# Kernel tuning notes

Hardware: AMD Instinct MI355X
Metric: run time of the kernel (lower is better)

Reference implementation:

```python
import jax, jax.numpy as jnp
from jax import lax
import numpy as np

STATE_DIM = 64
CHANNELS = 128
SEQ_LEN = 4096
BATCH = 16
DT_MIN, DT_MAX = 1e-3, 1e-1


def hippo(n):
    # HiPPO-LegS construction, matching the torch staticmethod
    ar = jnp.arange(n, dtype=jnp.float32)
    P = jnp.sqrt(1.0 + 2.0 * ar)
    A = P[:, None] * P[None, :]
    A = jnp.tril(A) - jnp.diag(ar)
    B = jnp.sqrt(2.0 * ar + 1.0)
    return -A, B[:, None]


def setup_inputs() -> dict:
    key = jax.random.key(0)
    k_u, k_c = jax.random.split(key)
    A, B = hippo(STATE_DIM)
    # xavier_normal_ for C: std = sqrt(2/(fan_in+fan_out))
    std = float(np.sqrt(2.0 / (CHANNELS + STATE_DIM)))
    C = jax.random.normal(k_c, (CHANNELS, STATE_DIM), dtype=jnp.float32) * std
    D = jnp.ones((CHANNELS, 1), dtype=jnp.float32)
    # deterministic dt at log-midpoint of [dt_min, dt_max]
    dt = jnp.exp(jnp.array([(np.log(DT_MIN) + np.log(DT_MAX)) / 2.0], dtype=jnp.float32))
    u = jax.random.normal(k_u, (BATCH, SEQ_LEN), dtype=jnp.float32)
    return {"u": u, "A": A, "B": B, "C": C, "D": D, "dt": dt}


def reference(u, A, B, C, D, dt):
    # Training-path forward of LinearStateSpaceLayer (conv-kernel construction + conv1d)
    b, L = u.shape
    n = A.shape[0]
    dt_s = dt[0]
    I = jnp.eye(n, dtype=A.dtype)
    BL = jnp.linalg.inv(I - 0.5 * dt_s * A)            # bilinear discretization
    A_bar = BL @ (I + 0.5 * dt_s * A)                  # (n, n)
    B_bar = (BL * dt_s) @ B                            # (n, 1)

    # kernel k[j] = C @ A_bar^j @ B_bar for j = 0..L-1, via a scan of matvecs
    def step(v, _):
        return A_bar @ v, v
    _, vs = lax.scan(step, B_bar[:, 0], None, length=L)  # (L, n), vs[j] = A_bar^j B_bar
    k_causal = vs @ C.T                                  # (L, channels)
    # torch ordering: k_conv[c, 0, i] = C A_bar^{L-1-i} B_bar = k_causal[L-1-i, c]
    k_conv = k_causal[::-1].T[:, None, :]                # (channels, 1, L)

    # torch F.conv1d is cross-correlation; lax conv_general_dilated matches
    y = lax.conv_general_dilated(
        u[:, None, :], k_conv,
        window_strides=(1,), padding=[(L - 1, L - 1)],
        dimension_numbers=("NCH", "OIH", "NCH"),
    )[:, :, :L]                                          # (b, channels, L)

    # skip term: (u.unsqueeze(-1) @ D.T).transpose(-1,-2) == u[b,t] * D[c,0]
    y = y + u[:, None, :] * D[None, :, :]                # (b, channels, L)
    return y
```

## Files before the change

### kernel.cpp

```cpp
#include <hip/hip_runtime.h>

#define NS   64
#define CH   128
#define LSEQ 4096
#define NB   16
#define SCH  64
#define MCH  64
#define ST   68
#define CP   128

#define WS_ABAR 0
#define WS_A16  4096
#define WS_VS   8192
#define WS_BBAR 12288

#define X0_IDX(b, m) (((size_t)(b) * CH) * LSEQ + (size_t)(m) * SCH)

#define P_VSS  0
#define P_XCW  1024
#define P_XBS  1280
#define P_PLE  1536
#define P_PART 1792
#define P_A16  2048

#define FMA44(av, bv)                                                          \
    a0.x += av.x * bv.x; a0.y += av.x * bv.y; a0.z += av.x * bv.z; a0.w += av.x * bv.w; \
    a1.x += av.y * bv.x; a1.y += av.y * bv.y; a1.z += av.y * bv.z; a1.w += av.y * bv.w; \
    a2.x += av.z * bv.x; a2.y += av.z * bv.y; a2.z += av.z * bv.z; a2.w += av.z * bv.w; \
    a3.x += av.w * bv.x; a3.y += av.w * bv.y; a3.z += av.w * bv.z; a3.w += av.w * bv.w;

template<bool WT>
__device__ __forceinline__ void mm_square(const float* __restrict__ cm,
                                          const float* __restrict__ cmt,
                                          float* __restrict__ nm,
                                          float* __restrict__ nmt, int e) {
    const int l = e & 63;
    const int si0 = 16 * ((e >> 6) & 3) + 4 * (l >> 4);
    const int sj0 = 4 * (l & 15);
    float4 a0 = {0,0,0,0}, a1 = {0,0,0,0}, a2 = {0,0,0,0}, a3 = {0,0,0,0};
#pragma unroll 4
    for (int k = 0; k < NS; k += 4) {
        float4 av0 = *(const float4*)&cmt[(k + 0) * ST + si0];
        float4 bv0 = *(const float4*)&cm [(k + 0) * ST + sj0];
        float4 av1 = *(const float4*)&cmt[(k + 1) * ST + si0];
        float4 bv1 = *(const float4*)&cm [(k + 1) * ST + sj0];
        float4 av2 = *(const float4*)&cmt[(k + 2) * ST + si0];
        float4 bv2 = *(const float4*)&cm [(k + 2) * ST + sj0];
        float4 av3 = *(const float4*)&cmt[(k + 3) * ST + si0];
        float4 bv3 = *(const float4*)&cm [(k + 3) * ST + sj0];
        FMA44(av0, bv0)
        FMA44(av1, bv1)
        FMA44(av2, bv2)
        FMA44(av3, bv3)
    }
    *(float4*)&nm[(si0 + 0) * ST + sj0] = a0;
    *(float4*)&nm[(si0 + 1) * ST + sj0] = a1;
    *(float4*)&nm[(si0 + 2) * ST + sj0] = a2;
    *(float4*)&nm[(si0 + 3) * ST + sj0] = a3;
    if (WT) {
        float4 t0 = {a0.x, a1.x, a2.x, a3.x};
        float4 t1 = {a0.y, a1.y, a2.y, a3.y};
        float4 t2 = {a0.z, a1.z, a2.z, a3.z};
        float4 t3 = {a0.w, a1.w, a2.w, a3.w};
        *(float4*)&nmt[(sj0 + 0) * ST + si0] = t0;
        *(float4*)&nmt[(sj0 + 1) * ST + si0] = t1;
        *(float4*)&nmt[(sj0 + 2) * ST + si0] = t2;
        *(float4*)&nmt[(sj0 + 3) * ST + si0] = t3;
    }
}

template<int R>
__device__ __forceinline__ void horner_step(const float* __restrict__ Acol,
                                            const float* __restrict__ xle,
                                            const float* __restrict__ Hprev,
                                            float* __restrict__ Hcur, int e) {
    const int g = e >> 4, i0 = 4 * (e & 15);
    const float* bp = (R == 1) ? &xle[(4 * g) * NS] : &Hprev[g * ST];
    float4 acc = *(const float4*)&xle[(4 * g + R) * NS + i0];
#pragma unroll 8
    for (int k = 0; k < NS; ++k) {
        float4 av = *(const float4*)&Acol[k * ST + i0];
        float bk = bp[k];
        acc.x = fmaf(av.x, bk, acc.x); acc.y = fmaf(av.y, bk, acc.y);
        acc.z = fmaf(av.z, bk, acc.z); acc.w = fmaf(av.w, bk, acc.w);
    }
    *(float4*)&Hcur[g * ST + i0] = acc;
}

__device__ __forceinline__ void inner_step(const float* __restrict__ Acol,
                                           const float* __restrict__ xle,
                                           float* __restrict__ stash, int r, int e) {
    const int g = e >> 4, i0 = 4 * (e & 15);
    const int mp = 4 * g + r - 1;
    float4 acc = *(const float4*)&xle[mp * NS + i0];
    const float* xp = &stash[mp * ST];
#pragma unroll 8
    for (int k = 0; k < NS; ++k) {
        float4 av = *(const float4*)&Acol[k * ST + i0];
        float xk = xp[k];
        acc.x = fmaf(av.x, xk, acc.x); acc.y = fmaf(av.y, xk, acc.y);
        acc.z = fmaf(av.z, xk, acc.z); acc.w = fmaf(av.w, xk, acc.w);
    }
    *(float4*)&stash[(mp + 1) * ST + i0] = acc;
}

__global__ __launch_bounds__(512) void k_sb(const float* __restrict__ u,
                                            const float* __restrict__ A,
                                            const float* __restrict__ Bv,
                                            const float* __restrict__ dtp,
                                            float* __restrict__ ws,
                                            float* __restrict__ out) {
    __shared__ __align__(16) float Mrow[NS * ST];
    __shared__ __align__(16) float Mcol[(NS + 1) * ST];
    __shared__ __align__(16) float Nrow[NS * ST];
    __shared__ __align__(16) float Ncol[NS * ST];
    __shared__ __align__(16) float VT[NS * ST];
    __shared__ __align__(16) float uT[NS * ST];
    __shared__ __align__(16) float vsS[NS * NS];
    __shared__ __align__(16) float xleS[MCH * NS];
    __shared__ __align__(16) float part[2][4 * NS];
    __shared__ __align__(16) float bcol[NS];
    __shared__ float rdiag[NS], xcS[NS];
    float* const stash = uT;
    float* const Hb0 = vsS;
    float* const Hb1 = vsS + 16 * ST;
    const int tid = threadIdx.x;
    const int b = blockIdx.x;
    const float dt = dtp[0];
    const float hdt = 0.5f * dt;

    for (int o = tid; o < NS * NS; o += 512) {
        int i = o >> 6, k = o & 63;
        float a = A[o];
        float d = (i == k) ? 1.0f : 0.0f;
        Nrow[i * ST + k] = d - hdt * a;
        Ncol[k * ST + i] = d + hdt * a;
    }
    if (tid < NS) {
        bcol[tid]  = dt * Bv[tid];
        rdiag[tid] = 1.0f / (1.0f - hdt * A[tid * NS + tid]);
    }
    __syncthreads();

    {
        const int jj = tid & 63;
#pragma unroll
        for (int rep = 0; rep < 2; ++rep) {
            const int m0 = 4 * (tid >> 6) + 32 * rep;
            float4 v;
            v.x = u[b * LSEQ + (m0 + 0) * SCH + 63 - jj];
            v.y = u[b * LSEQ + (m0 + 1) * SCH + 63 - jj];
            v.z = u[b * LSEQ + (m0 + 2) * SCH + 63 - jj];
            v.w = u[b * LSEQ + (m0 + 3) * SCH + 63 - jj];
            *(float4*)&uT[jj * ST + m0] = v;
        }
    }

    if (tid <= NS) {
        float xr[NS];
        const float* t2b = (tid < NS) ? &Ncol[tid * ST] : bcol;
#pragma unroll
        for (int I = 0; I < 16; ++I) {
            const int i0 = 4 * I;
            float4 t2 = *(const float4*)&t2b[i0];
            float a0 = t2.x, a1 = t2.y, a2 = t2.z, a3 = t2.w;
#pragma unroll
            for (int k = 0; k < i0; k += 4) {
                float4 n0 = *(const float4*)&Nrow[(i0 + 0) * ST + k];
                float4 n1 = *(const float4*)&Nrow[(i0 + 1) * ST + k];
                float4 n2 = *(const float4*)&Nrow[(i0 + 2) * ST + k];
                float4 n3 = *(const float4*)&Nrow[(i0 + 3) * ST + k];
                a0 -= n0.x * xr[k] + n0.y * xr[k + 1] + n0.z * xr[k + 2] + n0.w * xr[k + 3];
                a1 -= n1.x * xr[k] + n1.y * xr[k + 1] + n1.z * xr[k + 2] + n1.w * xr[k + 3];
                a2 -= n2.x * xr[k] + n2.y * xr[k + 1] + n2.z * xr[k + 2] + n2.w * xr[k + 3];
                a3 -= n3.x * xr[k] + n3.y * xr[k + 1] + n3.z * xr[k + 2] + n3.w * xr[k + 3];
            }
            float4 rd  = *(const float4*)&rdiag[i0];
            float4 nb1 = *(const float4*)&Nrow[(i0 + 1) * ST + i0];
            float4 nb2 = *(const float4*)&Nrow[(i0 + 2) * ST + i0];
            float4 nb3 = *(const float4*)&Nrow[(i0 + 3) * ST + i0];
            float x0 = a0 * rd.x;
            float x1 = (a1 - nb1.x * x0) * rd.y;
            float x2 = (a2 - nb2.x * x0 - nb2.y * x1) * rd.z;
            float x3 = (a3 - nb3.x * x0 - nb3.y * x1 - nb3.z * x2) * rd.w;
            xr[i0 + 0] = x0; xr[i0 + 1] = x1; xr[i0 + 2] = x2; xr[i0 + 3] = x3;
        }
        float* xrow = &Mcol[tid * ST];
#pragma unroll
        for (int k = 0; k < NS; k += 4) {
            float4 v = {xr[k], xr[k + 1], xr[k + 2], xr[k + 3]};
            *(float4*)&xrow[k] = v;
        }
    }
    __syncthreads();

    if (tid < 256) {
        const int i0 = 4 * (tid >> 4), j0 = 4 * (tid & 15);
        float4 r0 = *(const float4*)&Mcol[(j0 + 0) * ST + i0];
        float4 r1 = *(const float4*)&Mcol[(j0 + 1) * ST + i0];
        float4 r2 = *(const float4*)&Mcol[(j0 + 2) * ST + i0];
        float4 r3 = *(const float4*)&Mcol[(j0 + 3) * ST + i0];
        float4 w0 = {r0.x, r1.x, r2.x, r3.x};
        float4 w1 = {r0.y, r1.y, r2.y, r3.y};
        float4 w2 = {r0.z, r1.z, r2.z, r3.z};
        float4 w3 = {r0.w, r1.w, r2.w, r3.w};
        *(float4*)&Mrow[(i0 + 0) * ST + j0] = w0;
        *(float4*)&Mrow[(i0 + 1) * ST + j0] = w1;
        *(float4*)&Mrow[(i0 + 2) * ST + j0] = w2;
        *(float4*)&Mrow[(i0 + 3) * ST + j0] = w3;
        if (b == 0) {
            *(float4*)&ws[WS_ABAR + (i0 + 0) * NS + j0] = w0;
            *(float4*)&ws[WS_ABAR + (i0 + 1) * NS + j0] = w1;
            *(float4*)&ws[WS_ABAR + (i0 + 2) * NS + j0] = w2;
            *(float4*)&ws[WS_ABAR + (i0 + 3) * NS + j0] = w3;
        }
    }
    if (b == 0 && tid < 16)
        *(float4*)&ws[WS_BBAR + 4 * tid] = *(const float4*)&Mcol[NS * ST + 4 * tid];
    if (tid < NS) VT[tid * ST + 0] = Mcol[NS * ST + tid];
    __syncthreads();

    float *cm = Mrow, *cmt = Mcol, *nm = Nrow, *nmt = Ncol;
    for (int s = 1; s <= 6; ++s) {
        if (tid < 256) {
            mm_square<true>(cm, cmt, nm, nmt, tid);
        } else {
            const int e = tid - 256;
            if (s == 1) {
                if (e < NS) {
                    float sum = 0.f;
#pragma unroll 8
                    for (int k = 0; k < NS; ++k) sum += cmt[k * ST + e] * VT[k * ST + 0];
                    VT[e * ST + 1] = sum;
                }
            } else if (s == 2) {
                if (e < 2 * NS) {
                    const int i = e & 63, j = e >> 6;
                    float sum = 0.f;
#pragma unroll 8
                    for (int k = 0; k < NS; ++k) sum += cmt[k * ST + i] * VT[k * ST + j];
                    VT[i * ST + 2 + j] = sum;
                }
            } else {
                const int mexp = 1 << (s - 1);
                if (e < 4 * mexp) {
                    const int vi = 4 * (e & 15), vj = 4 * (e >> 4);
                    float4 a0 = {0,0,0,0}, a1 = {0,0,0,0}, a2 = {0,0,0,0}, a3 = {0,0,0,0};
#pragma unroll 4
                    for (int k = 0; k < NS; k += 2) {
                        float4 av  = *(const float4*)&cmt[k * ST + vi];
                        float4 bv  = *(const float4*)&VT [k * ST + vj];
                        float4 av2 = *(const float4*)&cmt[(k + 1) * ST + vi];
                        float4 bv2 = *(const float4*)&VT [(k + 1) * ST + vj];
                        FMA44(av, bv)
                        FMA44(av2, bv2)
                    }
                    *(float4*)&VT[(vi + 0) * ST + vj + mexp] = a0;
                    *(float4*)&VT[(vi + 1) * ST + vj + mexp] = a1;
                    *(float4*)&VT[(vi + 2) * ST + vj + mexp] = a2;
                    *(float4*)&VT[(vi + 3) * ST + vj + mexp] = a3;
                }
            }
        }
        __syncthreads();
        { float* t = cm; cm = nm; nm = t; t = cmt; cmt = nmt; nmt = t; }
        if (s == 4 && b == 0) {
            for (int o = tid; o < (NS * NS) / 4; o += 512) {
                int r = o >> 4, c4 = (o & 15) * 4;
                *(float4*)&ws[WS_A16 + r * NS + c4] = *(const float4*)&cm[r * ST + c4];
            }
        }
    }

    if (tid < 256) {
        const int i0 = 4 * (tid >> 4), j0 = 4 * (tid & 15);
        float4 v0 = *(const float4*)&VT[(i0 + 0) * ST + j0];
        float4 v1 = *(const float4*)&VT[(i0 + 1) * ST + j0];
        float4 v2 = *(const float4*)&VT[(i0 + 2) * ST + j0];
        float4 v3 = *(const float4*)&VT[(i0 + 3) * ST + j0];
        float4 w0 = {v0.x, v1.x, v2.x, v3.x};
        float4 w1 = {v0.y, v1.y, v2.y, v3.y};
        float4 w2 = {v0.z, v1.z, v2.z, v3.z};
        float4 w3 = {v0.w, v1.w, v2.w, v3.w};
        *(float4*)&vsS[(j0 + 0) * NS + i0] = w0;
        *(float4*)&vsS[(j0 + 1) * NS + i0] = w1;
        *(float4*)&vsS[(j0 + 2) * NS + i0] = w2;
        *(float4*)&vsS[(j0 + 3) * NS + i0] = w3;
        if (b == 0) {
            *(float4*)&ws[WS_VS + (j0 + 0) * NS + i0] = w0;
            *(float4*)&ws[WS_VS + (j0 + 1) * NS + i0] = w1;
            *(float4*)&ws[WS_VS + (j0 + 2) * NS + i0] = w2;
            *(float4*)&ws[WS_VS + (j0 + 3) * NS + i0] = w3;
        }
    } else {
        mm_square<true>(Mrow, Mcol, Nrow, Ncol, tid - 256);
    }
    __syncthreads();

    if (tid < 256) {
        const int ig = tid & 15, mg = tid >> 4;
        float4 a0 = {0,0,0,0}, a1 = {0,0,0,0}, a2 = {0,0,0,0}, a3 = {0,0,0,0};
#pragma unroll 4
        for (int j = 0; j < NS; j += 2) {
            float4 am  = *(const float4*)&uT[j * ST + 4 * mg];
            float4 bi  = *(const float4*)&vsS[j * NS + 4 * ig];
            float4 am2 = *(const float4*)&uT[(j + 1) * ST + 4 * mg];
            float4 bi2 = *(const float4*)&vsS[(j + 1) * NS + 4 * ig];
            FMA44(am, bi)
            FMA44(am2, bi2)
        }
        *(float4*)&xleS[(4 * mg + 0) * NS + 4 * ig] = a0;
        *(float4*)&xleS[(4 * mg + 1) * NS + 4 * ig] = a1;
        *(float4*)&xleS[(4 * mg + 2) * NS + 4 * ig] = a2;
        *(float4*)&xleS[(4 * mg + 3) * NS + 4 * ig] = a3;
    } else {
        mm_square<false>(Nrow, Ncol, VT, VT, tid - 256);
    }
    __syncthreads();

    float4 a256[4];
    if (tid < 256) {
        const int i = tid & 63, q = tid >> 6;
#pragma unroll
        for (int kq = 0; kq < 4; ++kq)
            a256[kq] = *(const float4*)&VT[i * ST + 16 * q + 4 * kq];
        horner_step<1>(Mcol, xleS, Hb0, Hb0, tid);
    } else if (tid < 320) {
        xcS[tid - 256] = 0.f;
        stash[tid - 256] = 0.f;
    }
    __syncthreads();
    if (tid < 256) horner_step<2>(Mcol, xleS, Hb0, Hb1, tid);
    __syncthreads();
    if (tid < 256) horner_step<3>(Mcol, xleS, Hb1, Hb0, tid);
    __syncthreads();

    {
        const int i = tid & 63, q = (tid >> 6) & 3;
        for (int g = 0; g < 15; ++g) {
            if (tid < 256) {
                float4 t0 = *(const float4*)(xcS + 16 * q + 0);
                float4 t1 = *(const float4*)(xcS + 16 * q + 4);
                float4 t2 = *(const float4*)(xcS + 16 * q + 8);
                float4 t3 = *(const float4*)(xcS + 16 * q + 12);
                float s = a256[0].x * t0.x + a256[0].y * t0.y + a256[0].z * t0.z + a256[0].w * t0.w
                        + a256[1].x * t1.x + a256[1].y * t1.y + a256[1].z * t1.z + a256[1].w * t1.w
                        + a256[2].x * t2.x + a256[2].y * t2.y + a256[2].z * t2.z + a256[2].w * t2.w
                        + a256[3].x * t3.x + a256[3].y * t3.y + a256[3].z * t3.z + a256[3].w * t3.w;
                part[g & 1][q * 64 + i] = s;
            }
            __syncthreads();
            if (tid < 256) {
                float xn = part[g & 1][i] + part[g & 1][64 + i] + part[g & 1][128 + i]
                         + part[g & 1][192 + i] + Hb0[g * ST + i];
                xcS[i] = xn;
                stash[(4 * g + 4) * ST + i] = xn;
            }
        }
    }
    __syncthreads();

    for (int r = 1; r <= 3; ++r) {
        if (tid < 256) inner_step(Mcol, xleS, stash, r, tid);
        __syncthreads();
    }

    {
        const int m = tid >> 3, t8 = (tid & 7) * 8;
        float4 o1 = *(const float4*)&stash[m * ST + t8];
        float4 o2 = *(const float4*)&stash[m * ST + t8 + 4];
        *(float4*)&out[X0_IDX(b, m) + t8]     = o1;
        *(float4*)&out[X0_IDX(b, m) + t8 + 4] = o2;
    }
}

__global__ __launch_bounds__(256) void k_main2(const float* __restrict__ u,
                                               const float* __restrict__ Cm,
                                               const float* __restrict__ Dv,
                                               const float* __restrict__ ws,
                                               float* __restrict__ out) {
    __shared__ __align__(16) float Xl[NS * ST];
    __shared__ __align__(16) float pool[NS * CP];
    __shared__ float uS[SCH], DS[CH], bbS[NS];
    const int m = blockIdx.x, b = blockIdx.y;
    const int tid = threadIdx.x;
    const int l = tid & 63, w = tid >> 6;

    for (int o = tid; o < (NS * NS) / 4; o += 256) {
        int r = o >> 4, c4 = (o & 15) * 4;
        *(float4*)&Xl[r * ST + c4]          = *(const float4*)&ws[WS_ABAR + r * NS + c4];
        *(float4*)&pool[P_A16 + r * NS + c4] = *(const float4*)&ws[WS_A16 + r * NS + c4];
    }
    for (int o = tid; o < 16 * NS; o += 256) pool[P_VSS + o] = ws[WS_VS + o];
    if (tid < NS) {
        uS[tid]  = u[b * LSEQ + m * SCH + tid];
        bbS[tid] = ws[WS_BBAR + tid];
        pool[P_XBS + tid] = out[X0_IDX(b, m) + tid];
    }
    if (tid < CH) DS[tid] = Dv[tid];
    __syncthreads();

    const int r0 = l & 15, q = l >> 4;
    float4 ar[4][4];
#pragma unroll
    for (int b4 = 0; b4 < 4; ++b4)
#pragma unroll
        for (int kq = 0; kq < 4; ++kq)
            ar[b4][kq] = *(const float4*)&Xl[(r0 + 16 * b4) * ST + 16 * q + 4 * kq];
    float bbr[4];
#pragma unroll
    for (int b4 = 0; b4 < 4; ++b4) bbr[b4] = bbS[r0 + 16 * b4];
    float4 a16r[4];
#pragma unroll
    for (int kq = 0; kq < 4; ++kq)
        a16r[kq] = *(const float4*)&pool[P_A16 + l * NS + 16 * w + 4 * kq];

    {
        float s = 0.f;
#pragma unroll
        for (int j = 0; j < 16; ++j) s += pool[P_VSS + j * NS + l] * uS[16 * w + 15 - j];
        pool[P_PLE + w * NS + l] = s;
    }
    __syncthreads();

    for (int p = 1; p < 4; ++p) {
        float4 x0q = *(const float4*)&pool[P_XBS + (p - 1) * NS + 16 * w + 0];
        float4 x1q = *(const float4*)&pool[P_XBS + (p - 1) * NS + 16 * w + 4];
        float4 x2q = *(const float4*)&pool[P_XBS + (p - 1) * NS + 16 * w + 8];
        float4 x3q = *(const float4*)&pool[P_XBS + (p - 1) * NS + 16 * w + 12];
        float s = a16r[0].x * x0q.x + a16r[0].y * x0q.y + a16r[0].z * x0q.z + a16r[0].w * x0q.w
                + a16r[1].x * x1q.x + a16r[1].y * x1q.y + a16r[1].z * x1q.z + a16r[1].w * x1q.w
                + a16r[2].x * x2q.x + a16r[2].y * x2q.y + a16r[2].z * x2q.z + a16r[2].w * x2q.w
                + a16r[3].x * x3q.x + a16r[3].y * x3q.y + a16r[3].z * x3q.z + a16r[3].w * x3q.w;
        pool[P_PART + w * NS + l] = s;
        __syncthreads();
        if (w == 0) {
            float xn = pool[P_PART + l] + pool[P_PART + NS + l] + pool[P_PART + 2 * NS + l]
                     + pool[P_PART + 3 * NS + l] + pool[P_PLE + (p - 1) * NS + l];
            pool[P_XBS + p * NS + l] = xn;
        }
        __syncthreads();
    }

    pool[P_XCW + w * NS + l] = pool[P_XBS + w * NS + l];
    for (int s = 0; s < 16; ++s) {
        __threadfence_block();
        const int t = 16 * w + s;
        float4 x0q = *(const float4*)&pool[P_XCW + w * NS + 16 * q + 0];
        float4 x1q = *(const float4*)&pool[P_XCW + w * NS + 16 * q + 4];
        float4 x2q = *(const float4*)&pool[P_XCW + w * NS + 16 * q + 8];
        float4 x3q = *(const float4*)&pool[P_XCW + w * NS + 16 * q + 12];
        float p0, p1, p2, p3;
        p0 = ar[0][0].x * x0q.x + ar[0][0].y * x0q.y + ar[0][0].z * x0q.z + ar[0][0].w * x0q.w
           + ar[0][1].x * x1q.x + ar[0][1].y * x1q.y + ar[0][1].z * x1q.z + ar[0][1].w * x1q.w
           + ar[0][2].x * x2q.x + ar[0][2].y * x2q.y + ar[0][2].z * x2q.z + ar[0][2].w * x2q.w
           + ar[0][3].x * x3q.x + ar[0][3].y * x3q.y + ar[0][3].z * x3q.z + ar[0][3].w * x3q.w;
        p1 = ar[1][0].x * x0q.x + ar[1][0].y * x0q.y + ar[1][0].z * x0q.z + ar[1][0].w * x0q.w
           + ar[1][1].x * x1q.x + ar[1][1].y * x1q.y + ar[1][1].z * x1q.z + ar[1][1].w * x1q.w
           + ar[1][2].x * x2q.x + ar[1][2].y * x2q.y + ar[1][2].z * x2q.z + ar[1][2].w * x2q.w
           + ar[1][3].x * x3q.x + ar[1][3].y * x3q.y + ar[1][3].z * x3q.z + ar[1][3].w * x3q.w;
        p2 = ar[2][0].x * x0q.x + ar[2][0].y * x0q.y + ar[2][0].z * x0q.z + ar[2][0].w * x0q.w
           + ar[2][1].x * x1q.x + ar[2][1].y * x1q.y + ar[2][1].z * x1q.z + ar[2][1].w * x1q.w
           + ar[2][2].x * x2q.x + ar[2][2].y * x2q.y + ar[2][2].z * x2q.z + ar[2][2].w * x2q.w
           + ar[2][3].x * x3q.x + ar[2][3].y * x3q.y + ar[2][3].z * x3q.z + ar[2][3].w * x3q.w;
        p3 = ar[3][0].x * x0q.x + ar[3][0].y * x0q.y + ar[3][0].z * x0q.z + ar[3][0].w * x0q.w
           + ar[3][1].x * x1q.x + ar[3][1].y * x1q.y + ar[3][1].z * x1q.z + ar[3][1].w * x1q.w
           + ar[3][2].x * x2q.x + ar[3][2].y * x2q.y + ar[3][2].z * x2q.z + ar[3][2].w * x2q.w
           + ar[3][3].x * x3q.x + ar[3][3].y * x3q.y + ar[3][3].z * x3q.z + ar[3][3].w * x3q.w;
        p0 += __shfl_xor(p0, 16, 64); p1 += __shfl_xor(p1, 16, 64);
        p2 += __shfl_xor(p2, 16, 64); p3 += __shfl_xor(p3, 16, 64);
        p0 += __shfl_xor(p0, 32, 64); p1 += __shfl_xor(p1, 32, 64);
        p2 += __shfl_xor(p2, 32, 64); p3 += __shfl_xor(p3, 32, 64);
        const float ut = uS[t];
        p0 += bbr[0] * ut; p1 += bbr[1] * ut; p2 += bbr[2] * ut; p3 += bbr[3] * ut;
        const float xv = (q == 0) ? p0 : (q == 1) ? p1 : (q == 2) ? p2 : p3;
        const int row = r0 + 16 * q;
        pool[P_XCW + w * NS + row] = xv;
        Xl[row * ST + t] = xv;
    }
    __syncthreads();

#pragma unroll
    for (int rep = 0; rep < 8; ++rep) {
        const int ii = tid & 63;
        const int cg = (tid >> 6) + 4 * rep;
        float4 v;
        v.x = Cm[(4 * cg + 0) * NS + ii];
        v.y = Cm[(4 * cg + 1) * NS + ii];
        v.z = Cm[(4 * cg + 2) * NS + ii];
        v.w = Cm[(4 * cg + 3) * NS + ii];
        *(float4*)&pool[ii * CP + 4 * cg] = v;
    }
    __syncthreads();

    {
        const int tg = tid & 7, cq = tid >> 3;
        float acc[4][8];
#pragma unroll
        for (int r = 0; r < 4; ++r)
#pragma unroll
            for (int c = 0; c < 8; ++c) acc[r][c] = 0.f;
#pragma unroll 4
        for (int ii = 0; ii < NS; ++ii) {
            float4 cv = *(const float4*)&pool[ii * CP + 4 * cq];
            float4 xa = *(const float4*)&Xl[ii * ST + 8 * tg + 0];
            float4 xb = *(const float4*)&Xl[ii * ST + 8 * tg + 4];
            float cr[4] = {cv.x, cv.y, cv.z, cv.w};
            float xv[8] = {xa.x, xa.y, xa.z, xa.w, xb.x, xb.y, xb.z, xb.w};
#pragma unroll
            for (int r = 0; r < 4; ++r)
#pragma unroll
                for (int c = 0; c < 8; ++c) acc[r][c] += cr[r] * xv[c];
        }
        const size_t obase = ((size_t)b * CH) * LSEQ + (size_t)m * SCH + 8 * tg;
#pragma unroll
        for (int r = 0; r < 4; ++r) {
            const int c = 4 * cq + r;
            const float dv = DS[c];
            float4 o1, o2;
            o1.x = acc[r][0] + dv * uS[8 * tg + 0];
            o1.y = acc[r][1] + dv * uS[8 * tg + 1];
            o1.z = acc[r][2] + dv * uS[8 * tg + 2];
            o1.w = acc[r][3] + dv * uS[8 * tg + 3];
            o2.x = acc[r][4] + dv * uS[8 * tg + 4];
            o2.y = acc[r][5] + dv * uS[8 * tg + 5];
            o2.z = acc[r][6] + dv * uS[8 * tg + 6];
            o2.w = acc[r][7] + dv * uS[8 * tg + 7];
            float* op = out + obase + (size_t)c * LSEQ;
            *(float4*)(op)     = o1;
            *(float4*)(op + 4) = o2;
        }
    }
}

extern "C" void kernel_launch(void* const* d_in, const int* in_sizes, int n_in,
                              void* d_out, int out_size, void* d_ws, size_t ws_size,
                              hipStream_t stream) {
    const float* u   = (const float*)d_in[0];
    const float* A   = (const float*)d_in[1];
    const float* Bv  = (const float*)d_in[2];
    const float* Cm  = (const float*)d_in[3];
    const float* Dv  = (const float*)d_in[4];
    const float* dtp = (const float*)d_in[5];
    float* ws  = (float*)d_ws;
    float* out = (float*)d_out;

    k_sb<<<NB, 512, 0, stream>>>(u, A, Bv, dtp, ws, out);
    k_main2<<<dim3(MCH, NB), 256, 0, stream>>>(u, Cm, Dv, ws, out);
}
```

Measured before the change: 156.6 us.

## Spread squaring and Horner steps across all 512 threads to shorten serial chain

Early matrix-squaring steps now use all 512 threads with a 4x2 tile, so the power-vector expansion runs alongside instead of in a separate half of the block. The three-step Horner recurrence is reorganised into two independent pair products followed by a combine using a squared matrix, which removes one barrier-separated serial step. The inner fill-in steps are likewise split across both thread halves using the squared matrix. This aims to cut latency in a single-block-per-batch setup-bound kernel, at the cost of extra FLOPs and reliance on the squared-matrix buffer holding the right power.

New measurement: 154.3 us. No clear change (-1.5%).

```diff
diff --git a/kernel.cpp b/kernel.cpp
--- a/kernel.cpp
+++ b/kernel.cpp
@@ -69,14 +69,56 @@
     }
 }
 
-template<int R>
-__device__ __forceinline__ void horner_step(const float* __restrict__ Acol,
-                                            const float* __restrict__ xle,
-                                            const float* __restrict__ Hprev,
-                                            float* __restrict__ Hcur, int e) {
+__device__ __forceinline__ void mm_sq42(const float* __restrict__ cm,
+                                        const float* __restrict__ cmt,
+                                        float* __restrict__ nm,
+                                        float* __restrict__ nmt, int tid) {
+    const int si0 = 4 * (tid >> 5);
+    const int sj0 = 2 * (tid & 31);
+    float2 a0 = {0,0}, a1 = {0,0}, a2 = {0,0}, a3 = {0,0};
+#pragma unroll 8
+    for (int k = 0; k < NS; ++k) {
+        float4 av = *(const float4*)&cmt[k * ST + si0];
+        float2 bv = *(const float2*)&cm [k * ST + sj0];
+        a0.x += av.x * bv.x; a0.y += av.x * bv.y;
+        a1.x += av.y * bv.x; a1.y += av.y * bv.y;
+        a2.x += av.z * bv.x; a2.y += av.z * bv.y;
+        a3.x += av.w * bv.x; a3.y += av.w * bv.y;
+    }
+    *(float2*)&nm[(si0 + 0) * ST + sj0] = a0;
+    *(float2*)&nm[(si0 + 1) * ST + sj0] = a1;
+    *(float2*)&nm[(si0 + 2) * ST + sj0] = a2;
+    *(float2*)&nm[(si0 + 3) * ST + sj0] = a3;
+    float4 t0 = {a0.x, a1.x, a2.x, a3.x};
+    float4 t1 = {a0.y, a1.y, a2.y, a3.y};
+    *(float4*)&nmt[(sj0 + 0) * ST + si0] = t0;
+    *(float4*)&nmt[(sj0 + 1) * ST + si0] = t1;
+}
+
+__device__ __forceinline__ void vs_expand1(const float* __restrict__ cmt,
+                                           float* __restrict__ VT,
+                                           int iq, int j, int mexp) {
+    const int i0 = 4 * iq;
+    float4 acc = {0,0,0,0};
+#pragma unroll 8
+    for (int k = 0; k < NS; ++k) {
+        float4 av = *(const float4*)&cmt[k * ST + i0];
+        float bk = VT[k * ST + j];
+        acc.x += av.x * bk; acc.y += av.y * bk;
+        acc.z += av.z * bk; acc.w += av.w * bk;
+    }
+    VT[(i0 + 0) * ST + mexp + j] = acc.x;
+    VT[(i0 + 1) * ST + mexp + j] = acc.y;
+    VT[(i0 + 2) * ST + mexp + j] = acc.z;
+    VT[(i0 + 3) * ST + mexp + j] = acc.w;
+}
+
+__device__ __forceinline__ void pq_step(const float* __restrict__ Acol,
+                                        const float* __restrict__ xle,
+                                        float* __restrict__ outb, int r0, int e) {
     const int g = e >> 4, i0 = 4 * (e & 15);
-    const float* bp = (R == 1) ? &xle[(4 * g) * NS] : &Hprev[g * ST];
-    float4 acc = *(const float4*)&xle[(4 * g + R) * NS + i0];
+    const float* bp = &xle[(4 * g + r0) * NS];
+    float4 acc = *(const float4*)&xle[(4 * g + r0 + 1) * NS + i0];
 #pragma unroll 8
     for (int k = 0; k < NS; ++k) {
         float4 av = *(const float4*)&Acol[k * ST + i0];
@@ -84,7 +126,24 @@
         acc.x = fmaf(av.x, bk, acc.x); acc.y = fmaf(av.y, bk, acc.y);
         acc.z = fmaf(av.z, bk, acc.z); acc.w = fmaf(av.w, bk, acc.w);
     }
-    *(float4*)&Hcur[g * ST + i0] = acc;
+    *(float4*)&outb[g * ST + i0] = acc;
+}
+
+__device__ __forceinline__ void y_step(const float* __restrict__ A128col,
+                                       const float* __restrict__ P,
+                                       const float* __restrict__ Q,
+                                       float* __restrict__ Y, int e) {
+    const int g = e >> 4, i0 = 4 * (e & 15);
+    const float* bp = &P[g * ST];
+    float4 acc = *(const float4*)&Q[g * ST + i0];
+#pragma unroll 8
+    for (int k = 0; k < NS; ++k) {
+        float4 av = *(const float4*)&A128col[k * ST + i0];
+        float bk = bp[k];
+        acc.x = fmaf(av.x, bk, acc.x); acc.y = fmaf(av.y, bk, acc.y);
+        acc.z = fmaf(av.z, bk, acc.z); acc.w = fmaf(av.w, bk, acc.w);
+    }
+    *(float4*)&Y[g * ST + i0] = acc;
 }
 
 __device__ __forceinline__ void inner_step(const float* __restrict__ Acol,
@@ -102,6 +161,22 @@
         acc.z = fmaf(av.z, xk, acc.z); acc.w = fmaf(av.w, xk, acc.w);
     }
     *(float4*)&stash[(mp + 1) * ST + i0] = acc;
+}
+
+__device__ __forceinline__ void e1u_step(const float* __restrict__ A128col,
+                                         const float* __restrict__ P,
+                                         float* __restrict__ stash, int e) {
+    const int g = e >> 4, i0 = 4 * (e & 15);
+    const float* xp = &stash[(4 * g) * ST];
+    float4 acc = *(const float4*)&P[g * ST + i0];
+#pragma unroll 8
+    for (int k = 0; k < NS; ++k) {
+        float4 av = *(const float4*)&A128col[k * ST + i0];
+        float xk = xp[k];
+        acc.x = fmaf(av.x, xk, acc.x); acc.y = fmaf(av.y, xk, acc.y);
+        acc.z = fmaf(av.z, xk, acc.z); acc.w = fmaf(av.w, xk, acc.w);
+    }
+    *(float4*)&stash[(4 * g + 2) * ST + i0] = acc;
 }
 
 __global__ __launch_bounds__(512) void k_sb(const float* __restrict__ u,
@@ -122,8 +197,9 @@
     __shared__ __align__(16) float bcol[NS];
     __shared__ float rdiag[NS], xcS[NS];
     float* const stash = uT;
-    float* const Hb0 = vsS;
-    float* const Hb1 = vsS + 16 * ST;
+    float* const HbP = vsS;
+    float* const HbQ = vsS + 16 * ST;
+    float* const HbY = vsS + 32 * ST;
     const int tid = threadIdx.x;
     const int b = blockIdx.x;
     const float dt = dtp[0];
@@ -222,44 +298,38 @@
 
     float *cm = Mrow, *cmt = Mcol, *nm = Nrow, *nmt = Ncol;
     for (int s = 1; s <= 6; ++s) {
-        if (tid < 256) {
+        if (s <= 4) {
+            mm_sq42(cm, cmt, nm, nmt, tid);
+            const int mexp = 1 << (s - 1);
+            if (tid < 16 * mexp) {
+                vs_expand1(cmt, VT, tid & 15, tid >> 4, mexp);
+            }
+        } else if (tid < 256) {
             mm_square<true>(cm, cmt, nm, nmt, tid);
         } else {
             const int e = tid - 256;
-            if (s == 1) {
-                if (e < NS) {
-                    float sum = 0.f;
+            const int iq = e & 15;
+            if (s == 5) {
+                vs_expand1(cmt, VT, iq, e >> 4, 16);
+            } else {
+                const int j0 = 2 * (e >> 4);
+                const int i0 = 4 * iq;
+                float4 c0 = {0,0,0,0}, c1 = {0,0,0,0};
 #pragma unroll 8
-                    for (int k = 0; k < NS; ++k) sum += cmt[k * ST + e] * VT[k * ST + 0];
-                    VT[e * ST + 1] = sum;
+                for (int k = 0; k < NS; ++k) {
+                    float4 av = *(const float4*)&cmt[k * ST + i0];
+                    float2 bv = *(const float2*)&VT[k * ST + j0];
+                    c0.x += av.x * bv.x; c0.y += av.y * bv.x;
+                    c0.z += av.z * bv.x; c0.w += av.w * bv.x;
+                    c1.x += av.x * bv.y; c1.y += av.y * bv.y;
+                    c1.z += av.z * bv.y; c1.w += av.w * bv.y;
                 }
-            } else if (s == 2) {
-                if (e < 2 * NS) {
-                    const int i = e & 63, j = e >> 6;
-                    float sum = 0.f;
-#pragma unroll 8
-                    for (int k = 0; k < NS; ++k) sum += cmt[k * ST + i] * VT[k * ST + j];
-                    VT[i * ST + 2 + j] = sum;
-                }
-            } else {
-                const int mexp = 1 << (s - 1);
-                if (e < 4 * mexp) {
-                    const int vi = 4 * (e & 15), vj = 4 * (e >> 4);
-                    float4 a0 = {0,0,0,0}, a1 = {0,0,0,0}, a2 = {0,0,0,0}, a3 = {0,0,0,0};
-#pragma unroll 4
-                    for (int k = 0; k < NS; k += 2) {
-                        float4 av  = *(const float4*)&cmt[k * ST + vi];
-                        float4 bv  = *(const float4*)&VT [k * ST + vj];
-                        float4 av2 = *(const float4*)&cmt[(k + 1) * ST + vi];
-                        float4 bv2 = *(const float4*)&VT [(k + 1) * ST + vj];
-                        FMA44(av, bv)
-                        FMA44(av2, bv2)
-                    }
-                    *(float4*)&VT[(vi + 0) * ST + vj + mexp] = a0;
-                    *(float4*)&VT[(vi + 1) * ST + vj + mexp] = a1;
-                    *(float4*)&VT[(vi + 2) * ST + vj + mexp] = a2;
-                    *(float4*)&VT[(vi + 3) * ST + vj + mexp] = a3;
-                }
+                float2 w0 = {c0.x, c1.x}, w1 = {c0.y, c1.y};
+                float2 w2 = {c0.z, c1.z}, w3 = {c0.w, c1.w};
+                *(float2*)&VT[(i0 + 0) * ST + 32 + j0] = w0;
+                *(float2*)&VT[(i0 + 1) * ST + 32 + j0] = w1;
+                *(float2*)&VT[(i0 + 2) * ST + 32 + j0] = w2;
+                *(float2*)&VT[(i0 + 3) * ST + 32 + j0] = w3;
             }
         }
         __syncthreads();
@@ -324,15 +394,18 @@
 #pragma unroll
         for (int kq = 0; kq < 4; ++kq)
             a256[kq] = *(const float4*)&VT[i * ST + 16 * q + 4 * kq];
-        horner_step<1>(Mcol, xleS, Hb0, Hb0, tid);
+        pq_step(Mcol, xleS, HbP, 0, tid);
+    } else {
+        pq_step(Mcol, xleS, HbQ, 2, tid - 256);
+    }
+    __syncthreads();
+
+    if (tid < 256) {
+        y_step(Ncol, HbP, HbQ, HbY, tid);
     } else if (tid < 320) {
         xcS[tid - 256] = 0.f;
         stash[tid - 256] = 0.f;
     }
-    __syncthreads();
-    if (tid < 256) horner_step<2>(Mcol, xleS, Hb0, Hb1, tid);
-    __syncthreads();
-    if (tid < 256) horner_step<3>(Mcol, xleS, Hb1, Hb0, tid);
     __syncthreads();
 
     {
@@ -352,7 +425,7 @@
             __syncthreads();
             if (tid < 256) {
                 float xn = part[g & 1][i] + part[g & 1][64 + i] + part[g & 1][128 + i]
-                         + part[g & 1][192 + i] + Hb0[g * ST + i];
+                         + part[g & 1][192 + i] + HbY[g * ST + i];
                 xcS[i] = xn;
                 stash[(4 * g + 4) * ST + i] = xn;
             }
@@ -360,10 +433,12 @@
     }
     __syncthreads();
 
-    for (int r = 1; r <= 3; ++r) {
-        if (tid < 256) inner_step(Mcol, xleS, stash, r, tid);
-        __syncthreads();
-    }
+    if (tid < 256) inner_step(Mcol, xleS, stash, 1, tid);
+    else           e1u_step(Ncol, HbP, stash, tid - 256);
+    __syncthreads();
+
+    if (tid < 256) inner_step(Mcol, xleS, stash, 3, tid);
+    __syncthreads();
 
     {
         const int m = tid >> 3, t8 = (tid & 7) * 8;
```
